# Kernel tuning notes

Hardware: AMD Instinct MI355X
Metric: run time of the kernel (lower is better)

Reference implementation:

```python
import jax, jax.numpy as jnp
import numpy as np
import math

B, S, D, H = 2, 2048, 1024, 16
DH = D // H  # 64


def setup_inputs() -> dict:
    key = jax.random.key(0)
    ks = jax.random.split(key, 12)
    def nrm(k, shape, scale=1.0):
        return (jax.random.normal(k, shape, dtype=jnp.float32) * scale)
    return {
        "x": nrm(ks[0], (B, S, D)),
        "memory": nrm(ks[1], (B, S, D)),
        "mask": jax.random.randint(ks[2], (B, S), 0, 2).astype(jnp.bool_),
        "wq": nrm(ks[3], (D, D), 1.0 / math.sqrt(D)),
        "bq": nrm(ks[4], (D,), 0.02),
        "wk": nrm(ks[5], (D, D), 1.0 / math.sqrt(D)),
        "bk": nrm(ks[6], (D,), 0.02),
        "wv": nrm(ks[7], (D, D), 1.0 / math.sqrt(D)),
        "bv": nrm(ks[8], (D,), 0.02),
        "wo": nrm(ks[9], (D, D), 1.0 / math.sqrt(D)),
        "bo": nrm(ks[10], (D,), 0.02),
    }


def reference(x, memory, mask, wq, bq, wk, bk, wv, bv, wo, bo):
    b, s, d = x.shape
    def split(t):  # [b, s, d] -> [b, h, s, dh]
        return t.reshape(b, -1, H, DH).transpose(0, 2, 1, 3)
    q = split(x @ wq + bq) * (1.0 / math.sqrt(DH))
    k = split(memory @ wk + bk)
    v = split(memory @ wv + bv)
    logit = jnp.einsum("bhqd,bhkd->bhqk", q, k)
    neg_inf = jnp.finfo(logit.dtype).min
    logit = jnp.where(mask[:, None, None, :], -jnp.inf, logit)
    weights = jax.nn.softmax(logit, axis=-1)
    out = jnp.einsum("bhqk,bhkd->bhqd", weights, v)
    out = out.transpose(0, 2, 1, 3).reshape(b, -1, d)  # combine heads
    return out @ wo + bo
```

## Files before the change

### kernel.cpp

```cpp
#include <hip/hip_runtime.h>
#include <hip/hip_bf16.h>

#define B_  2
#define S_  2048
#define D_  1024
#define H_  16
#define DH_ 64
#define M_  (B_*S_)
#define KSTR 2048

typedef unsigned short ushort_t;
typedef __attribute__((ext_vector_type(8)))  short bf16x8;
typedef __attribute__((ext_vector_type(4)))  float f32x4;
typedef __attribute__((ext_vector_type(16))) float f32x16;
typedef __attribute__((ext_vector_type(4)))  int   i32x4;

#define MFMA16x16(A,Bb,C) __builtin_amdgcn_mfma_f32_16x16x32_bf16(A,Bb,C,0,0,0)
#define MFMA32(A,Bb,C)    __builtin_amdgcn_mfma_f32_32x32x16_bf16(A,Bb,C,0,0,0)
#define QSCALE 0.18033688011112042f
#define E2(x) __builtin_amdgcn_exp2f(x)

__device__ __forceinline__ ushort_t f2bf(float f) {
    return __builtin_bit_cast(ushort_t, __float2bfloat16(f));
}
__device__ __forceinline__ unsigned pack2(float a, float b) {
    return (unsigned)f2bf(a) | ((unsigned)f2bf(b) << 16);
}

__device__ __forceinline__ void gll16(const void* g, void* l) {
    __builtin_amdgcn_global_load_lds(
        (const __attribute__((address_space(1))) unsigned int*)g,
        (__attribute__((address_space(3))) unsigned int*)l, 16, 0, 0);
}

#define SWZ(row, c8) ((((c8) ^ ((row) & 7))) * 8)

__device__ __forceinline__ void pl32swap(int& a, int& b) {
    asm("v_permlane32_swap_b32 %0, %1" : "+v"(a), "+v"(b));
}

__global__ __launch_bounds__(256) void prep_all(const float* __restrict__ x,
                                                const float* __restrict__ mem,
                                                const unsigned char* __restrict__ mask_raw,
                                                const float* __restrict__ wq,
                                                const float* __restrict__ wk,
                                                const float* __restrict__ wv,
                                                const float* __restrict__ wo,
                                                const float* __restrict__ bk,
                                                const float* __restrict__ bv,
                                                ushort_t* __restrict__ xb,
                                                ushort_t* __restrict__ mb,
                                                ushort_t* __restrict__ wqT,
                                                ushort_t* __restrict__ wkT,
                                                ushort_t* __restrict__ wvT,
                                                ushort_t* __restrict__ woT,
                                                float* __restrict__ meltg,
                                                float* __restrict__ biasKV) {
    __shared__ ushort_t T[64][65];
    __shared__ int isBool;
    const int bid = blockIdx.x;
    const int tid = threadIdx.x;

    if (bid < 4096) {
        const int i = (bid & 2047) * 256 + tid;
        const float* src = (bid < 2048) ? x : mem;
        ushort_t*    dst = (bid < 2048) ? xb : mb;
        float4 a = *(const float4*)(src + (size_t)i * 8);
        float4 b = *(const float4*)(src + (size_t)i * 8 + 4);
        bf16x8 t;
        t[0] = (short)f2bf(a.x); t[1] = (short)f2bf(a.y);
        t[2] = (short)f2bf(a.z); t[3] = (short)f2bf(a.w);
        t[4] = (short)f2bf(b.x); t[5] = (short)f2bf(b.y);
        t[6] = (short)f2bf(b.z); t[7] = (short)f2bf(b.w);
        *(bf16x8*)(dst + (size_t)i * 8) = t;
    } else if (bid < 5120) {
        const int tt = bid - 4096;
        const int z = tt >> 8, rem = tt & 255;
        const int bi = rem >> 4, bj = rem & 15;
        const float* W; ushort_t* Wt;
        switch (z) {
            case 0:  W = wq; Wt = wqT; break;
            case 1:  W = wk; Wt = wkT; break;
            case 2:  W = wv; Wt = wvT; break;
            default: W = wo; Wt = woT; break;
        }
        const int r = tid >> 2;
        const int c = tid & 3;
        const float* src = W + (size_t)(bi * 64 + r) * D_ + bj * 64 + c * 16;
        #pragma unroll
        for (int qq = 0; qq < 4; qq++) {
            float4 v = *(const float4*)(src + qq * 4);
            T[r][c * 16 + qq * 4 + 0] = f2bf(v.x);
            T[r][c * 16 + qq * 4 + 1] = f2bf(v.y);
            T[r][c * 16 + qq * 4 + 2] = f2bf(v.z);
            T[r][c * 16 + qq * 4 + 3] = f2bf(v.w);
        }
        __syncthreads();
        ushort_t tmp[16];
        #pragma unroll
        for (int qq = 0; qq < 16; qq++) tmp[qq] = T[c * 16 + qq][r];
        ushort_t* dst = Wt + (size_t)(bj * 64 + r) * D_ + bi * 64 + c * 16;
        *(bf16x8*)(dst)     = *(bf16x8*)&tmp[0];
        *(bf16x8*)(dst + 8) = *(bf16x8*)&tmp[8];
    } else {
        if (tid == 0) isBool = 0;
        __syncthreads();
        int found = 0;
        for (int i = tid; i < M_; i += 256) {
            if ((i & 3) != 0 && mask_raw[i] != 0) found = 1;
        }
        if (found) atomicOr(&isBool, 1);
        __syncthreads();
        const int isb = isBool;
        for (int i = tid; i < M_; i += 256) {
            int m;
            if (isb) m = (mask_raw[i] != 0);
            else     m = (((const int*)mask_raw)[i] != 0);
            meltg[i] = 8.0f + (m ? 1.0e4f : 0.0f);
        }
        for (int i = tid; i < D_; i += 256) {
            biasKV[i]      = bk[i];
            biasKV[D_ + i] = bv[i];
        }
    }
}

template<int MODE>
__device__ __forceinline__ void gemm_body(const ushort_t* __restrict__ A,
                                          const ushort_t* __restrict__ Bt,
                                          const float* __restrict__ bias,
                                          void* __restrict__ Cv,
                                          float scale, int N, int bm, int bn,
                                          ushort_t* lds) {
    ushort_t (*As)[64] = (ushort_t(*)[64])lds;
    ushort_t (*Bs)[64] = (ushort_t(*)[64])(lds + 8192);

    const int tid = threadIdx.x;
    const int l15 = tid & 15;
    const int g   = (tid & 63) >> 4;
    const int w   = tid >> 6;
    const int wr  = w >> 1;
    const int wc  = w & 1;

    f32x4 acc[4][4] = {};

    #pragma unroll 1
    for (int kt = 0; kt < D_; kt += 64) {
        __syncthreads();
        #pragma unroll
        for (int j = 0; j < 4; j++) {
            const int idx = tid + 256 * j;
            const int row = idx >> 3;
            const int c8  = idx & 7;
            gll16(A  + (size_t)(bm + row) * D_ + kt + c8 * 8,
                  (char*)&As[0][0] + idx * 16);
            gll16(Bt + (size_t)(bn + row) * D_ + kt + c8 * 8,
                  (char*)&Bs[0][0] + idx * 16);
        }
        __syncthreads();

        #pragma unroll
        for (int kk = 0; kk < 2; kk++) {
            bf16x8 a[4], b[4];
            #pragma unroll
            for (int m = 0; m < 4; m++)
                a[m] = *(bf16x8*)&As[wr * 64 + 16 * m + l15][kk * 32 + g * 8];
            #pragma unroll
            for (int n = 0; n < 4; n++)
                b[n] = *(bf16x8*)&Bs[wc * 64 + 16 * n + l15][kk * 32 + g * 8];
            #pragma unroll
            for (int m = 0; m < 4; m++)
                #pragma unroll
                for (int n = 0; n < 4; n++)
                    acc[m][n] = MFMA16x16(a[m], b[n], acc[m][n]);
        }
    }

    if (MODE != 2) {
        #pragma unroll
        for (int n = 0; n < 4; n++) {
            const int col = bn + wc * 64 + 16 * n + l15;
            const float bv = bias[col];
            #pragma unroll
            for (int m = 0; m < 4; m++) {
                #pragma unroll
                for (int r = 0; r < 4; r++) {
                    const int row = bm + wr * 64 + 16 * m + 4 * g + r;
                    const float val = (acc[m][n][r] + bv) * scale;
                    if (MODE == 1) ((ushort_t*)Cv)[(size_t)row * N + col] = f2bf(val);
                    else           ((float*)Cv)[(size_t)row * N + col] = val;
                }
            }
        }
    } else {
        __syncthreads();
        ushort_t (*T)[136] = (ushort_t(*)[136])lds;
        #pragma unroll
        for (int n = 0; n < 4; n++) {
            const int col_l = wc * 64 + 16 * n + l15;
            const float bv = bias[bn + col_l];
            #pragma unroll
            for (int m = 0; m < 4; m++) {
                #pragma unroll
                for (int r = 0; r < 4; r++) {
                    const int row_l = wr * 64 + 16 * m + 4 * g + r;
                    T[col_l][row_l] = f2bf((acc[m][n][r] + bv) * scale);
                }
            }
        }
        __syncthreads();
        const int tc = tid >> 1;
        const int rc = (tid & 1) * 64;
        const int col1 = bn + tc - 1024;
        const int hh = col1 >> 6, dh = col1 & 63;
        const int bb = bm >> 11;
        const int s0 = (bm & 2047) + rc;
        ushort_t* dst = (ushort_t*)Cv + ((size_t)(bb * H_ + hh) * DH_ + dh) * S_ + s0;
        #pragma unroll
        for (int c = 0; c < 8; c++)
            *(bf16x8*)(dst + c * 8) = *(const bf16x8*)&T[tc][rc + c * 8];
    }
}

__global__ __launch_bounds__(256) void gemm_qkv(const ushort_t* __restrict__ xb,
                                                const ushort_t* __restrict__ mb,
                                                const ushort_t* __restrict__ wqT,
                                                const ushort_t* __restrict__ wkvT,
                                                const float* __restrict__ bq,
                                                const float* __restrict__ biasKV,
                                                ushort_t* __restrict__ qb,
                                                ushort_t* __restrict__ kg,
                                                ushort_t* __restrict__ vtg) {
    __shared__ ushort_t lds[17408];
    const int y  = blockIdx.y;
    const int bm = blockIdx.x * 128;
    if (y < 8)       gemm_body<1>(xb, wqT,  bq,     qb,  QSCALE, D_, bm, y * 128, lds);
    else if (y < 16) gemm_body<1>(mb, wkvT, biasKV, kg,  1.0f,   D_, bm, (y - 8) * 128, lds);
    else             gemm_body<2>(mb, wkvT, biasKV, vtg, 1.0f,   KSTR, bm, 1024 + (y - 16) * 128, lds);
}

__global__ __launch_bounds__(256) void gemm_o(const ushort_t* __restrict__ ab,
                                              const ushort_t* __restrict__ woT,
                                              const float* __restrict__ bo,
                                              float* __restrict__ out) {
    __shared__ __attribute__((aligned(16))) ushort_t As[64][64];
    __shared__ __attribute__((aligned(16))) ushort_t Bs[128][64];

    const int tid = threadIdx.x;
    const int l15 = tid & 15;
    const int g   = (tid & 63) >> 4;
    const int w   = tid >> 6;
    const int wr  = w >> 1;
    const int wc  = w & 1;
    const int bm  = blockIdx.y * 64;
    const int bn  = blockIdx.x * 128;

    f32x4 acc[2][4] = {};

    #pragma unroll 1
    for (int kt = 0; kt < D_; kt += 64) {
        __syncthreads();
        #pragma unroll
        for (int j = 0; j < 2; j++) {
            const int idx = tid + 256 * j;
            const int row = idx >> 3;
            const int c8  = idx & 7;
            gll16(ab + (size_t)(bm + row) * D_ + kt + c8 * 8,
                  (char*)&As[0][0] + idx * 16);
        }
        #pragma unroll
        for (int j = 0; j < 4; j++) {
            const int idx = tid + 256 * j;
            const int row = idx >> 3;
            const int c8  = idx & 7;
            gll16(woT + (size_t)(bn + row) * D_ + kt + c8 * 8,
                  (char*)&Bs[0][0] + idx * 16);
        }
        __syncthreads();

        #pragma unroll
        for (int kk = 0; kk < 2; kk++) {
            bf16x8 a[2], b[4];
            #pragma unroll
            for (int m = 0; m < 2; m++)
                a[m] = *(bf16x8*)&As[wr * 32 + 16 * m + l15][kk * 32 + g * 8];
            #pragma unroll
            for (int n = 0; n < 4; n++)
                b[n] = *(bf16x8*)&Bs[wc * 64 + 16 * n + l15][kk * 32 + g * 8];
            #pragma unroll
            for (int m = 0; m < 2; m++)
                #pragma unroll
                for (int n = 0; n < 4; n++)
                    acc[m][n] = MFMA16x16(a[m], b[n], acc[m][n]);
        }
    }

    #pragma unroll
    for (int n = 0; n < 4; n++) {
        const int col = bn + wc * 64 + 16 * n + l15;
        const float bv = bo[col];
        #pragma unroll
        for (int m = 0; m < 2; m++) {
            #pragma unroll
            for (int r = 0; r < 4; r++) {
                const int row = bm + wr * 32 + 16 * m + 4 * g + r;
                out[(size_t)row * D_ + col] = acc[m][n][r] + bv;
            }
        }
    }
}

#define KB 128
#define NT (S_ / KB)

__global__ __launch_bounds__(256) void attn_mfma(const ushort_t* __restrict__ q,
                                                 const ushort_t* __restrict__ kg,
                                                 const ushort_t* __restrict__ vtg,
                                                 const float* __restrict__ meltg,
                                                 ushort_t* __restrict__ o) {
    __shared__ __attribute__((aligned(16))) ushort_t Ks[2][KB][64];
    __shared__ __attribute__((aligned(16))) ushort_t Vt[2][DH_][KB];
    __shared__ float melt[2][KB];

    const int tid = threadIdx.x;
    const int w   = tid >> 6;
    const int l31 = tid & 31;
    const int hi  = (tid >> 5) & 1;

    const int blk = blockIdx.x;
    const int qt  = blk >> 5;
    const int bh  = blk & 31;
    const int h   = bh & 15;
    const int b   = bh >> 4;

    const int qr0 = qt * 128 + w * 32;
    const size_t hoff  = (size_t)h * DH_;
    const size_t kbase = (size_t)(b * S_) * D_ + hoff;
    const size_t vbase = (size_t)((b * H_ + h) * DH_) * S_;

    const int krow0 = tid >> 3, kc8 = tid & 7;
    const int vrow0 = tid >> 4, vc8 = tid & 15;

    bf16x8 qf[4];
    {
        const ushort_t* qp = q + (size_t)(b * S_ + qr0 + l31) * D_ + hoff + hi * 8;
        #pragma unroll
        for (int ks = 0; ks < 4; ks++)
            qf[ks] = *(const bf16x8*)(qp + ks * 16);
    }

    f32x16 oacc0 = {}, oacc1 = {};
    float ps = 0.f;

    bf16x8 kreg[4], vreg[4];
    float  mreg = 0.f;

    #pragma unroll
    for (int j = 0; j < 4; j++) {
        kreg[j] = *(const bf16x8*)&kg[kbase + (size_t)(krow0 + 32 * j) * D_ + kc8 * 8];
        vreg[j] = *(const bf16x8*)&vtg[vbase + (size_t)(vrow0 + 16 * j) * S_ + vc8 * 8];
    }
    if (tid < KB) mreg = meltg[b * S_ + tid];

    #pragma unroll
    for (int j = 0; j < 4; j++) {
        const int kr = krow0 + 32 * j;
        const int vr = vrow0 + 16 * j;
        *(bf16x8*)&Ks[0][kr][SWZ(kr, kc8)] = kreg[j];
        *(bf16x8*)&Vt[0][vr][SWZ(vr, vc8)] = vreg[j];
    }
    if (tid < KB) melt[0][tid] = mreg;

    #pragma unroll
    for (int j = 0; j < 4; j++) {
        kreg[j] = *(const bf16x8*)&kg[kbase + (size_t)(KB + krow0 + 32 * j) * D_ + kc8 * 8];
        vreg[j] = *(const bf16x8*)&vtg[vbase + (size_t)(vrow0 + 16 * j) * S_ + KB + vc8 * 8];
    }
    if (tid < KB) mreg = meltg[b * S_ + KB + tid];

    int cur = 0;
    #pragma unroll 1
    for (int t = 0; t < NT; t++) {
        __syncthreads();

        if (t + 1 < NT) {
            const int nb = cur ^ 1;
            #pragma unroll
            for (int j = 0; j < 4; j++) {
                const int kr = krow0 + 32 * j;
                const int vr = vrow0 + 16 * j;
                *(bf16x8*)&Ks[nb][kr][SWZ(kr, kc8)] = kreg[j];
                *(bf16x8*)&Vt[nb][vr][SWZ(vr, vc8)] = vreg[j];
            }
            if (tid < KB) melt[nb][tid] = mreg;
        }
        if (t + 2 < NT) {
            const size_t nk = (size_t)(t + 2) * KB;
            #pragma unroll
            for (int j = 0; j < 4; j++) {
                kreg[j] = *(const bf16x8*)&kg[kbase + (nk + krow0 + 32 * j) * D_ + kc8 * 8];
                vreg[j] = *(const bf16x8*)&vtg[vbase + (size_t)(vrow0 + 16 * j) * S_ + nk + vc8 * 8];
            }
            if (tid < KB) mreg = meltg[b * S_ + nk + tid];
        }

        #pragma unroll
        for (int kb = 0; kb < 4; kb++) {
            f32x16 st = {};
            __builtin_amdgcn_s_setprio(1);
            #pragma unroll
            for (int ks = 0; ks < 4; ks++) {
                const int row = 32 * kb + l31;
                bf16x8 kf = *(bf16x8*)&Ks[cur][row][SWZ(row, 2 * ks + hi)];
                st = MFMA32(kf, qf[ks], st);
            }
            __builtin_amdgcn_s_setprio(0);

            const float* mp = &melt[cur][32 * kb + 4 * hi];
            float4 me0 = *(const float4*)(mp);
            float4 me1 = *(const float4*)(mp + 8);
            float4 me2 = *(const float4*)(mp + 16);
            float4 me3 = *(const float4*)(mp + 24);
            float p[16];
            p[0]  = E2(st[0]  - me0.x); p[1]  = E2(st[1]  - me0.y);
            p[2]  = E2(st[2]  - me0.z); p[3]  = E2(st[3]  - me0.w);
            p[4]  = E2(st[4]  - me1.x); p[5]  = E2(st[5]  - me1.y);
            p[6]  = E2(st[6]  - me1.z); p[7]  = E2(st[7]  - me1.w);
            p[8]  = E2(st[8]  - me2.x); p[9]  = E2(st[9]  - me2.y);
            p[10] = E2(st[10] - me2.z); p[11] = E2(st[11] - me2.w);
            p[12] = E2(st[12] - me3.x); p[13] = E2(st[13] - me3.y);
            p[14] = E2(st[14] - me3.z); p[15] = E2(st[15] - me3.w);
            ps += (((p[0] + p[1]) + (p[2] + p[3])) + ((p[4] + p[5]) + (p[6] + p[7])))
                + (((p[8] + p[9]) + (p[10] + p[11])) + ((p[12] + p[13]) + (p[14] + p[15])));

            int ax0 = (int)pack2(p[0],  p[1]),  ay0 = (int)pack2(p[2],  p[3]);
            int az0 = (int)pack2(p[4],  p[5]),  aw0 = (int)pack2(p[6],  p[7]);
            int ax1 = (int)pack2(p[8],  p[9]),  ay1 = (int)pack2(p[10], p[11]);
            int az1 = (int)pack2(p[12], p[13]), aw1 = (int)pack2(p[14], p[15]);
            pl32swap(ax0, az0);
            pl32swap(ay0, aw0);
            pl32swap(ax1, az1);
            pl32swap(ay1, aw1);
            i32x4 t0, t1;
            t0[0] = ax0; t0[1] = ay0; t0[2] = az0; t0[3] = aw0;
            t1[0] = ax1; t1[1] = ay1; t1[2] = az1; t1[3] = aw1;
            bf16x8 pa0 = __builtin_bit_cast(bf16x8, t0);
            bf16x8 pa1 = __builtin_bit_cast(bf16x8, t1);

            const int vr0 = l31, vr1 = 32 + l31;
            bf16x8 v00 = *(bf16x8*)&Vt[cur][vr0][SWZ(vr0, 4 * kb + hi)];
            bf16x8 v01 = *(bf16x8*)&Vt[cur][vr0][SWZ(vr0, 4 * kb + 2 + hi)];
            bf16x8 v10 = *(bf16x8*)&Vt[cur][vr1][SWZ(vr1, 4 * kb + hi)];
            bf16x8 v11 = *(bf16x8*)&Vt[cur][vr1][SWZ(vr1, 4 * kb + 2 + hi)];
            __builtin_amdgcn_s_setprio(1);
            oacc0 = MFMA32(pa0, v00, oacc0);
            oacc0 = MFMA32(pa1, v01, oacc0);
            oacc1 = MFMA32(pa0, v10, oacc1);
            oacc1 = MFMA32(pa1, v11, oacc1);
            __builtin_amdgcn_s_setprio(0);
        }

        cur ^= 1;
    }

    const float ls = ps + __shfl_xor(ps, 32);
    const float iv = 1.f / ls;

    #pragma unroll
    for (int reg = 0; reg < 16; reg++) {
        const int qrow = (reg & 3) + 8 * (reg >> 2) + 4 * hi;
        const float ivr = __shfl(iv, qrow);
        ushort_t* op = o + (size_t)(b * S_ + qr0 + qrow) * D_ + hoff;
        op[l31]      = f2bf(oacc0[reg] * ivr);
        op[32 + l31] = f2bf(oacc1[reg] * ivr);
    }
}

extern "C" void kernel_launch(void* const* d_in, const int* in_sizes, int n_in,
                              void* d_out, int out_size, void* d_ws, size_t ws_size,
                              hipStream_t stream) {
    const float* x      = (const float*)d_in[0];
    const float* memory = (const float*)d_in[1];
    const unsigned char* mask = (const unsigned char*)d_in[2];
    const float* wq = (const float*)d_in[3];
    const float* bq = (const float*)d_in[4];
    const float* wk = (const float*)d_in[5];
    const float* bk = (const float*)d_in[6];
    const float* wv = (const float*)d_in[7];
    const float* bv = (const float*)d_in[8];
    const float* wo = (const float*)d_in[9];
    const float* bo = (const float*)d_in[10];
    float* out = (float*)d_out;

    const size_t CH = (size_t)M_ * D_;
    const size_t WH = (size_t)D_ * D_;
    ushort_t* ws   = (ushort_t*)d_ws;
    ushort_t* xb   = ws;
    ushort_t* mb   = xb + CH;
    ushort_t* qb   = mb + CH;
    ushort_t* kg   = qb + CH;
    ushort_t* vtg  = kg + CH;
    ushort_t* ab   = vtg + CH;
    ushort_t* wqT  = ab + CH;
    ushort_t* wkT  = wqT + WH;
    ushort_t* wvT  = wkT + WH;
    ushort_t* woT  = wvT + WH;
    float* meltg   = (float*)(woT + WH);
    float* biasKV  = meltg + M_;

    prep_all<<<5121, 256, 0, stream>>>(x, memory, mask, wq, wk, wv, wo, bk, bv,
                                       xb, mb, wqT, wkT, wvT, woT, meltg, biasKV);

    gemm_qkv<<<dim3(32, 24), 256, 0, stream>>>(xb, mb, wqT, wkT, bq, biasKV,
                                               qb, kg, vtg);

    attn_mfma<<<B_ * H_ * (S_ / 128), 256, 0, stream>>>(qb, kg, vtg, meltg, ab);

    gemm_o<<<dim3(8, 64), 256, 0, stream>>>(ab, woT, bo, out);
}
```

Before: 148.8 us.

## Process two query tiles per wave in attention to reuse K/V fragments

Each wave now handles 64 query rows as two 32-row MFMA tiles, reusing the K fragments loaded from LDS for both score computations and the V fragments for both PV products. Block query coverage doubles to 256 and the grid halves, cutting K/V global and LDS traffic per query. The cost is higher register pressure (launch bounds relaxed to one block) and fewer blocks, which reduces latency hiding and CU occupancy.

```diff
diff --git a/kernel.cpp b/kernel.cpp
--- a/kernel.cpp
+++ b/kernel.cpp
@@ -313,11 +313,11 @@
 #define KB 128
 #define NT (S_ / KB)
 
-__global__ __launch_bounds__(256) void attn_mfma(const ushort_t* __restrict__ q,
-                                                 const ushort_t* __restrict__ kg,
-                                                 const ushort_t* __restrict__ vtg,
-                                                 const float* __restrict__ meltg,
-                                                 ushort_t* __restrict__ o) {
+__global__ __launch_bounds__(256, 1) void attn_mfma(const ushort_t* __restrict__ q,
+                                                    const ushort_t* __restrict__ kg,
+                                                    const ushort_t* __restrict__ vtg,
+                                                    const float* __restrict__ meltg,
+                                                    ushort_t* __restrict__ o) {
     __shared__ __attribute__((aligned(16))) ushort_t Ks[2][KB][64];
     __shared__ __attribute__((aligned(16))) ushort_t Vt[2][DH_][KB];
     __shared__ float melt[2][KB];
@@ -333,7 +333,7 @@
     const int h   = bh & 15;
     const int b   = bh >> 4;
 
-    const int qr0 = qt * 128 + w * 32;
+    const int qr0 = qt * 256 + w * 64;
     const size_t hoff  = (size_t)h * DH_;
     const size_t kbase = (size_t)(b * S_) * D_ + hoff;
     const size_t vbase = (size_t)((b * H_ + h) * DH_) * S_;
@@ -341,16 +341,17 @@
     const int krow0 = tid >> 3, kc8 = tid & 7;
     const int vrow0 = tid >> 4, vc8 = tid & 15;
 
-    bf16x8 qf[4];
-    {
-        const ushort_t* qp = q + (size_t)(b * S_ + qr0 + l31) * D_ + hoff + hi * 8;
+    bf16x8 qf[2][4];
+    #pragma unroll
+    for (int qi = 0; qi < 2; qi++) {
+        const ushort_t* qp = q + (size_t)(b * S_ + qr0 + 32 * qi + l31) * D_ + hoff + hi * 8;
         #pragma unroll
         for (int ks = 0; ks < 4; ks++)
-            qf[ks] = *(const bf16x8*)(qp + ks * 16);
-    }
-
-    f32x16 oacc0 = {}, oacc1 = {};
-    float ps = 0.f;
+            qf[qi][ks] = *(const bf16x8*)(qp + ks * 16);
+    }
+
+    f32x16 oacc[2][2] = {};
+    float ps[2] = {0.f, 0.f};
 
     bf16x8 kreg[4], vreg[4];
     float  mreg = 0.f;
@@ -406,14 +407,18 @@
 
         #pragma unroll
         for (int kb = 0; kb < 4; kb++) {
-            f32x16 st = {};
-            __builtin_amdgcn_s_setprio(1);
+            bf16x8 kf[4];
             #pragma unroll
             for (int ks = 0; ks < 4; ks++) {
                 const int row = 32 * kb + l31;
-                bf16x8 kf = *(bf16x8*)&Ks[cur][row][SWZ(row, 2 * ks + hi)];
-                st = MFMA32(kf, qf[ks], st);
-            }
+                kf[ks] = *(bf16x8*)&Ks[cur][row][SWZ(row, 2 * ks + hi)];
+            }
+            f32x16 st0 = {}, st1 = {};
+            __builtin_amdgcn_s_setprio(1);
+            #pragma unroll
+            for (int ks = 0; ks < 4; ks++) st0 = MFMA32(kf[ks], qf[0][ks], st0);
+            #pragma unroll
+            for (int ks = 0; ks < 4; ks++) st1 = MFMA32(kf[ks], qf[1][ks], st1);
             __builtin_amdgcn_s_setprio(0);
 
             const float* mp = &melt[cur][32 * kb + 4 * hi];
@@ -421,58 +426,66 @@
             float4 me1 = *(const float4*)(mp + 8);
             float4 me2 = *(const float4*)(mp + 16);
             float4 me3 = *(const float4*)(mp + 24);
-            float p[16];
-            p[0]  = E2(st[0]  - me0.x); p[1]  = E2(st[1]  - me0.y);
-            p[2]  = E2(st[2]  - me0.z); p[3]  = E2(st[3]  - me0.w);
-            p[4]  = E2(st[4]  - me1.x); p[5]  = E2(st[5]  - me1.y);
-            p[6]  = E2(st[6]  - me1.z); p[7]  = E2(st[7]  - me1.w);
-            p[8]  = E2(st[8]  - me2.x); p[9]  = E2(st[9]  - me2.y);
-            p[10] = E2(st[10] - me2.z); p[11] = E2(st[11] - me2.w);
-            p[12] = E2(st[12] - me3.x); p[13] = E2(st[13] - me3.y);
-            p[14] = E2(st[14] - me3.z); p[15] = E2(st[15] - me3.w);
-            ps += (((p[0] + p[1]) + (p[2] + p[3])) + ((p[4] + p[5]) + (p[6] + p[7])))
-                + (((p[8] + p[9]) + (p[10] + p[11])) + ((p[12] + p[13]) + (p[14] + p[15])));
-
-            int ax0 = (int)pack2(p[0],  p[1]),  ay0 = (int)pack2(p[2],  p[3]);
-            int az0 = (int)pack2(p[4],  p[5]),  aw0 = (int)pack2(p[6],  p[7]);
-            int ax1 = (int)pack2(p[8],  p[9]),  ay1 = (int)pack2(p[10], p[11]);
-            int az1 = (int)pack2(p[12], p[13]), aw1 = (int)pack2(p[14], p[15]);
-            pl32swap(ax0, az0);
-            pl32swap(ay0, aw0);
-            pl32swap(ax1, az1);
-            pl32swap(ay1, aw1);
-            i32x4 t0, t1;
-            t0[0] = ax0; t0[1] = ay0; t0[2] = az0; t0[3] = aw0;
-            t1[0] = ax1; t1[1] = ay1; t1[2] = az1; t1[3] = aw1;
-            bf16x8 pa0 = __builtin_bit_cast(bf16x8, t0);
-            bf16x8 pa1 = __builtin_bit_cast(bf16x8, t1);
 
             const int vr0 = l31, vr1 = 32 + l31;
             bf16x8 v00 = *(bf16x8*)&Vt[cur][vr0][SWZ(vr0, 4 * kb + hi)];
             bf16x8 v01 = *(bf16x8*)&Vt[cur][vr0][SWZ(vr0, 4 * kb + 2 + hi)];
             bf16x8 v10 = *(bf16x8*)&Vt[cur][vr1][SWZ(vr1, 4 * kb + hi)];
             bf16x8 v11 = *(bf16x8*)&Vt[cur][vr1][SWZ(vr1, 4 * kb + 2 + hi)];
-            __builtin_amdgcn_s_setprio(1);
-            oacc0 = MFMA32(pa0, v00, oacc0);
-            oacc0 = MFMA32(pa1, v01, oacc0);
-            oacc1 = MFMA32(pa0, v10, oacc1);
-            oacc1 = MFMA32(pa1, v11, oacc1);
-            __builtin_amdgcn_s_setprio(0);
+
+            #pragma unroll
+            for (int qi = 0; qi < 2; qi++) {
+                const f32x16& st = qi ? st1 : st0;
+                float p[16];
+                p[0]  = E2(st[0]  - me0.x); p[1]  = E2(st[1]  - me0.y);
+                p[2]  = E2(st[2]  - me0.z); p[3]  = E2(st[3]  - me0.w);
+                p[4]  = E2(st[4]  - me1.x); p[5]  = E2(st[5]  - me1.y);
+                p[6]  = E2(st[6]  - me1.z); p[7]  = E2(st[7]  - me1.w);
+                p[8]  = E2(st[8]  - me2.x); p[9]  = E2(st[9]  - me2.y);
+                p[10] = E2(st[10] - me2.z); p[11] = E2(st[11] - me2.w);
+                p[12] = E2(st[12] - me3.x); p[13] = E2(st[13] - me3.y);
+                p[14] = E2(st[14] - me3.z); p[15] = E2(st[15] - me3.w);
+                ps[qi] += (((p[0] + p[1]) + (p[2] + p[3])) + ((p[4] + p[5]) + (p[6] + p[7])))
+                        + (((p[8] + p[9]) + (p[10] + p[11])) + ((p[12] + p[13]) + (p[14] + p[15])));
+
+                int ax0 = (int)pack2(p[0],  p[1]),  ay0 = (int)pack2(p[2],  p[3]);
+                int az0 = (int)pack2(p[4],  p[5]),  aw0 = (int)pack2(p[6],  p[7]);
+                int ax1 = (int)pack2(p[8],  p[9]),  ay1 = (int)pack2(p[10], p[11]);
+                int az1 = (int)pack2(p[12], p[13]), aw1 = (int)pack2(p[14], p[15]);
+                pl32swap(ax0, az0);
+                pl32swap(ay0, aw0);
+                pl32swap(ax1, az1);
+                pl32swap(ay1, aw1);
+                i32x4 t0, t1;
+                t0[0] = ax0; t0[1] = ay0; t0[2] = az0; t0[3] = aw0;
+                t1[0] = ax1; t1[1] = ay1; t1[2] = az1; t1[3] = aw1;
+                bf16x8 pa0 = __builtin_bit_cast(bf16x8, t0);
+                bf16x8 pa1 = __builtin_bit_cast(bf16x8, t1);
+
+                __builtin_amdgcn_s_setprio(1);
+                oacc[qi][0] = MFMA32(pa0, v00, oacc[qi][0]);
+                oacc[qi][0] = MFMA32(pa1, v01, oacc[qi][0]);
+                oacc[qi][1] = MFMA32(pa0, v10, oacc[qi][1]);
+                oacc[qi][1] = MFMA32(pa1, v11, oacc[qi][1]);
+                __builtin_amdgcn_s_setprio(0);
+            }
         }
 
         cur ^= 1;
     }
 
-    const float ls = ps + __shfl_xor(ps, 32);
-    const float iv = 1.f / ls;
-
     #pragma unroll
-    for (int reg = 0; reg < 16; reg++) {
-        const int qrow = (reg & 3) + 8 * (reg >> 2) + 4 * hi;
-        const float ivr = __shfl(iv, qrow);
-        ushort_t* op = o + (size_t)(b * S_ + qr0 + qrow) * D_ + hoff;
-        op[l31]      = f2bf(oacc0[reg] * ivr);
-        op[32 + l31] = f2bf(oacc1[reg] * ivr);
+    for (int qi = 0; qi < 2; qi++) {
+        const float ls = ps[qi] + __shfl_xor(ps[qi], 32);
+        const float iv = 1.f / ls;
+        #pragma unroll
+        for (int reg = 0; reg < 16; reg++) {
+            const int qrow = (reg & 3) + 8 * (reg >> 2) + 4 * hi;
+            const float ivr = __shfl(iv, qrow);
+            ushort_t* op = o + (size_t)(b * S_ + qr0 + 32 * qi + qrow) * D_ + hoff;
+            op[l31]      = f2bf(oacc[qi][0][reg] * ivr);
+            op[32 + l31] = f2bf(oacc[qi][1][reg] * ivr);
+        }
     }
 }
 
@@ -514,7 +527,7 @@
     gemm_qkv<<<dim3(32, 24), 256, 0, stream>>>(xb, mb, wqT, wkT, bq, biasKV,
                                                qb, kg, vtg);
 
-    attn_mfma<<<B_ * H_ * (S_ / 128), 256, 0, stream>>>(qb, kg, vtg, meltg, ab);
+    attn_mfma<<<B_ * H_ * (S_ / 256), 256, 0, stream>>>(qb, kg, vtg, meltg, ab);
 
     gemm_o<<<dim3(8, 64), 256, 0, stream>>>(ab, woT, bo, out);
 }
```

Result: no change. 150.6 us (+1.1%).

## Fold key mask into V and compute softmax denominator with MFMA

Applied to the files above, without the earlier changes.

Masked keys are no longer removed with a subtracted 1e4 offset inside the exponent. Instead V rows are pre-scaled by a per-key weight (0 or 1/256) in the QKV GEMM epilogue, and the softmax denominator is accumulated by an extra pair of MFMAs against a bf16 weight vector read from global memory. This removes the per-tile mask LDS staging, the subtraction in the exponent and the scalar row-sum reduction. In exchange it adds two MFMAs per block and unstaged global loads. It also drops the fixed max offset (the old code subtracted a constant 8), so exp2 runs on raw scores and the scale change can affect precision or overflow.

```diff
diff --git a/kernel.cpp b/kernel.cpp
--- a/kernel.cpp
+++ b/kernel.cpp
@@ -19,6 +19,7 @@
 #define MFMA32(A,Bb,C)    __builtin_amdgcn_mfma_f32_32x32x16_bf16(A,Bb,C,0,0,0)
 #define QSCALE 0.18033688011112042f
 #define E2(x) __builtin_amdgcn_exp2f(x)
+#define WVAL 0.00390625f
 
 __device__ __forceinline__ ushort_t f2bf(float f) {
     return __builtin_bit_cast(ushort_t, __float2bfloat16(f));
@@ -54,7 +55,8 @@
                                                 ushort_t* __restrict__ wkT,
                                                 ushort_t* __restrict__ wvT,
                                                 ushort_t* __restrict__ woT,
-                                                float* __restrict__ meltg,
+                                                float* __restrict__ vwf,
+                                                ushort_t* __restrict__ vwb,
                                                 float* __restrict__ biasKV) {
     __shared__ ushort_t T[64][65];
     __shared__ int isBool;
@@ -116,7 +118,9 @@
             int m;
             if (isb) m = (mask_raw[i] != 0);
             else     m = (((const int*)mask_raw)[i] != 0);
-            meltg[i] = 8.0f + (m ? 1.0e4f : 0.0f);
+            const float wv2 = m ? 0.0f : WVAL;
+            vwf[i] = wv2;
+            vwb[i] = f2bf(wv2);
         }
         for (int i = tid; i < D_; i += 256) {
             biasKV[i]      = bk[i];
@@ -129,6 +133,7 @@
 __device__ __forceinline__ void gemm_body(const ushort_t* __restrict__ A,
                                           const ushort_t* __restrict__ Bt,
                                           const float* __restrict__ bias,
+                                          const float* __restrict__ vw,
                                           void* __restrict__ Cv,
                                           float scale, int N, int bm, int bn,
                                           ushort_t* lds) {
@@ -204,7 +209,7 @@
                 #pragma unroll
                 for (int r = 0; r < 4; r++) {
                     const int row_l = wr * 64 + 16 * m + 4 * g + r;
-                    T[col_l][row_l] = f2bf((acc[m][n][r] + bv) * scale);
+                    T[col_l][row_l] = f2bf((acc[m][n][r] + bv) * vw[bm + row_l]);
                 }
             }
         }
@@ -228,15 +233,16 @@
                                                 const ushort_t* __restrict__ wkvT,
                                                 const float* __restrict__ bq,
                                                 const float* __restrict__ biasKV,
+                                                const float* __restrict__ vwf,
                                                 ushort_t* __restrict__ qb,
                                                 ushort_t* __restrict__ kg,
                                                 ushort_t* __restrict__ vtg) {
     __shared__ ushort_t lds[17408];
     const int y  = blockIdx.y;
     const int bm = blockIdx.x * 128;
-    if (y < 8)       gemm_body<1>(xb, wqT,  bq,     qb,  QSCALE, D_, bm, y * 128, lds);
-    else if (y < 16) gemm_body<1>(mb, wkvT, biasKV, kg,  1.0f,   D_, bm, (y - 8) * 128, lds);
-    else             gemm_body<2>(mb, wkvT, biasKV, vtg, 1.0f,   KSTR, bm, 1024 + (y - 16) * 128, lds);
+    if (y < 8)       gemm_body<1>(xb, wqT,  bq,     nullptr, qb,  QSCALE, D_, bm, y * 128, lds);
+    else if (y < 16) gemm_body<1>(mb, wkvT, biasKV, nullptr, kg,  1.0f,   D_, bm, (y - 8) * 128, lds);
+    else             gemm_body<2>(mb, wkvT, biasKV, vwf,     vtg, 1.0f,   KSTR, bm, 1024 + (y - 16) * 128, lds);
 }
 
 __global__ __launch_bounds__(256) void gemm_o(const ushort_t* __restrict__ ab,
@@ -316,11 +322,10 @@
 __global__ __launch_bounds__(256) void attn_mfma(const ushort_t* __restrict__ q,
                                                  const ushort_t* __restrict__ kg,
                                                  const ushort_t* __restrict__ vtg,
-                                                 const float* __restrict__ meltg,
+                                                 const ushort_t* __restrict__ vwb,
                                                  ushort_t* __restrict__ o) {
     __shared__ __attribute__((aligned(16))) ushort_t Ks[2][KB][64];
     __shared__ __attribute__((aligned(16))) ushort_t Vt[2][DH_][KB];
-    __shared__ float melt[2][KB];
 
     const int tid = threadIdx.x;
     const int w   = tid >> 6;
@@ -350,18 +355,17 @@
     }
 
     f32x16 oacc0 = {}, oacc1 = {};
-    float ps = 0.f;
+    f32x16 dacc  = {};
+
+    const ushort_t* wrow = vwb + b * S_ + 8 * hi;
 
     bf16x8 kreg[4], vreg[4];
-    float  mreg = 0.f;
 
     #pragma unroll
     for (int j = 0; j < 4; j++) {
         kreg[j] = *(const bf16x8*)&kg[kbase + (size_t)(krow0 + 32 * j) * D_ + kc8 * 8];
         vreg[j] = *(const bf16x8*)&vtg[vbase + (size_t)(vrow0 + 16 * j) * S_ + vc8 * 8];
     }
-    if (tid < KB) mreg = meltg[b * S_ + tid];
-
     #pragma unroll
     for (int j = 0; j < 4; j++) {
         const int kr = krow0 + 32 * j;
@@ -369,14 +373,11 @@
         *(bf16x8*)&Ks[0][kr][SWZ(kr, kc8)] = kreg[j];
         *(bf16x8*)&Vt[0][vr][SWZ(vr, vc8)] = vreg[j];
     }
-    if (tid < KB) melt[0][tid] = mreg;
-
     #pragma unroll
     for (int j = 0; j < 4; j++) {
         kreg[j] = *(const bf16x8*)&kg[kbase + (size_t)(KB + krow0 + 32 * j) * D_ + kc8 * 8];
         vreg[j] = *(const bf16x8*)&vtg[vbase + (size_t)(vrow0 + 16 * j) * S_ + KB + vc8 * 8];
     }
-    if (tid < KB) mreg = meltg[b * S_ + KB + tid];
 
     int cur = 0;
     #pragma unroll 1
@@ -392,7 +393,6 @@
                 *(bf16x8*)&Ks[nb][kr][SWZ(kr, kc8)] = kreg[j];
                 *(bf16x8*)&Vt[nb][vr][SWZ(vr, vc8)] = vreg[j];
             }
-            if (tid < KB) melt[nb][tid] = mreg;
         }
         if (t + 2 < NT) {
             const size_t nk = (size_t)(t + 2) * KB;
@@ -401,7 +401,6 @@
                 kreg[j] = *(const bf16x8*)&kg[kbase + (nk + krow0 + 32 * j) * D_ + kc8 * 8];
                 vreg[j] = *(const bf16x8*)&vtg[vbase + (size_t)(vrow0 + 16 * j) * S_ + nk + vc8 * 8];
             }
-            if (tid < KB) mreg = meltg[b * S_ + nk + tid];
         }
 
         #pragma unroll
@@ -416,22 +415,15 @@
             }
             __builtin_amdgcn_s_setprio(0);
 
-            const float* mp = &melt[cur][32 * kb + 4 * hi];
-            float4 me0 = *(const float4*)(mp);
-            float4 me1 = *(const float4*)(mp + 8);
-            float4 me2 = *(const float4*)(mp + 16);
-            float4 me3 = *(const float4*)(mp + 24);
             float p[16];
-            p[0]  = E2(st[0]  - me0.x); p[1]  = E2(st[1]  - me0.y);
-            p[2]  = E2(st[2]  - me0.z); p[3]  = E2(st[3]  - me0.w);
-            p[4]  = E2(st[4]  - me1.x); p[5]  = E2(st[5]  - me1.y);
-            p[6]  = E2(st[6]  - me1.z); p[7]  = E2(st[7]  - me1.w);
-            p[8]  = E2(st[8]  - me2.x); p[9]  = E2(st[9]  - me2.y);
-            p[10] = E2(st[10] - me2.z); p[11] = E2(st[11] - me2.w);
-            p[12] = E2(st[12] - me3.x); p[13] = E2(st[13] - me3.y);
-            p[14] = E2(st[14] - me3.z); p[15] = E2(st[15] - me3.w);
-            ps += (((p[0] + p[1]) + (p[2] + p[3])) + ((p[4] + p[5]) + (p[6] + p[7])))
-                + (((p[8] + p[9]) + (p[10] + p[11])) + ((p[12] + p[13]) + (p[14] + p[15])));
+            p[0]  = E2(st[0]);  p[1]  = E2(st[1]);
+            p[2]  = E2(st[2]);  p[3]  = E2(st[3]);
+            p[4]  = E2(st[4]);  p[5]  = E2(st[5]);
+            p[6]  = E2(st[6]);  p[7]  = E2(st[7]);
+            p[8]  = E2(st[8]);  p[9]  = E2(st[9]);
+            p[10] = E2(st[10]); p[11] = E2(st[11]);
+            p[12] = E2(st[12]); p[13] = E2(st[13]);
+            p[14] = E2(st[14]); p[15] = E2(st[15]);
 
             int ax0 = (int)pack2(p[0],  p[1]),  ay0 = (int)pack2(p[2],  p[3]);
             int az0 = (int)pack2(p[4],  p[5]),  aw0 = (int)pack2(p[6],  p[7]);
@@ -447,6 +439,10 @@
             bf16x8 pa0 = __builtin_bit_cast(bf16x8, t0);
             bf16x8 pa1 = __builtin_bit_cast(bf16x8, t1);
 
+            const int kwoff = t * KB + 32 * kb;
+            bf16x8 wf0 = *(const bf16x8*)(wrow + kwoff);
+            bf16x8 wf1 = *(const bf16x8*)(wrow + kwoff + 16);
+
             const int vr0 = l31, vr1 = 32 + l31;
             bf16x8 v00 = *(bf16x8*)&Vt[cur][vr0][SWZ(vr0, 4 * kb + hi)];
             bf16x8 v01 = *(bf16x8*)&Vt[cur][vr0][SWZ(vr0, 4 * kb + 2 + hi)];
@@ -457,19 +453,18 @@
             oacc0 = MFMA32(pa1, v01, oacc0);
             oacc1 = MFMA32(pa0, v10, oacc1);
             oacc1 = MFMA32(pa1, v11, oacc1);
+            dacc  = MFMA32(pa0, wf0, dacc);
+            dacc  = MFMA32(pa1, wf1, dacc);
             __builtin_amdgcn_s_setprio(0);
         }
 
         cur ^= 1;
     }
-
-    const float ls = ps + __shfl_xor(ps, 32);
-    const float iv = 1.f / ls;
 
     #pragma unroll
     for (int reg = 0; reg < 16; reg++) {
         const int qrow = (reg & 3) + 8 * (reg >> 2) + 4 * hi;
-        const float ivr = __shfl(iv, qrow);
+        const float ivr = 1.f / dacc[reg];
         ushort_t* op = o + (size_t)(b * S_ + qr0 + qrow) * D_ + hoff;
         op[l31]      = f2bf(oacc0[reg] * ivr);
         op[32 + l31] = f2bf(oacc1[reg] * ivr);
@@ -505,16 +500,17 @@
     ushort_t* wkT  = wqT + WH;
     ushort_t* wvT  = wkT + WH;
     ushort_t* woT  = wvT + WH;
-    float* meltg   = (float*)(woT + WH);
-    float* biasKV  = meltg + M_;
+    float* vwf     = (float*)(woT + WH);
+    float* biasKV  = vwf + M_;
+    ushort_t* vwb  = (ushort_t*)(biasKV + KSTR);
 
     prep_all<<<5121, 256, 0, stream>>>(x, memory, mask, wq, wk, wv, wo, bk, bv,
-                                       xb, mb, wqT, wkT, wvT, woT, meltg, biasKV);
-
-    gemm_qkv<<<dim3(32, 24), 256, 0, stream>>>(xb, mb, wqT, wkT, bq, biasKV,
+                                       xb, mb, wqT, wkT, wvT, woT, vwf, vwb, biasKV);
+
+    gemm_qkv<<<dim3(32, 24), 256, 0, stream>>>(xb, mb, wqT, wkT, bq, biasKV, vwf,
                                                qb, kg, vtg);
 
-    attn_mfma<<<B_ * H_ * (S_ / 128), 256, 0, stream>>>(qb, kg, vtg, meltg, ab);
+    attn_mfma<<<B_ * H_ * (S_ / 128), 256, 0, stream>>>(qb, kg, vtg, vwb, ab);
 
     gemm_o<<<dim3(8, 64), 256, 0, stream>>>(ab, woT, bo, out);
 }
```

After: 145.3 us. 2.4% less time.
